# Performance work log

Hardware: AMD Instinct MI355X
Metric: run time of the kernel (lower is better)

## Reference

```python
import jax, jax.numpy as jnp
import numpy as np
from jax import lax

B, C, H, W = 2, 64, 96, 192
D = 48          # max_disp
G = 8           # num_groups
GC = C // G     # group channels
OUT = 32        # out_channels


def conv2d(x, w, pad):
    return lax.conv_general_dilated(x, w, (1, 1), [(pad, pad)] * 2,
                                    dimension_numbers=('NCHW', 'OIHW', 'NCHW'))


def conv3d(x, w, dil, pad):
    return lax.conv_general_dilated(x, w, (1, 1, 1), [(pad, pad)] * 3,
                                    rhs_dilation=(dil, dil, dil),
                                    dimension_numbers=('NCDHW', 'OIDHW', 'NCDHW'))


def setup_inputs() -> dict:
    key = jax.random.key(0)
    ks = jax.random.split(key, 9)
    s = 0.05
    return dict(
        feat_l=jax.random.normal(ks[0], (B, C, H, W), jnp.float32),
        feat_r=jax.random.normal(ks[1], (B, C, H, W), jnp.float32),
        edge_mask=jax.random.uniform(ks[2], (B, 1, H, W), jnp.float32),
        w_pred1=jax.random.normal(ks[3], (32, C + 1, 3, 3), jnp.float32) * s,
        bn_gamma=jnp.ones((32,), jnp.float32),
        bn_beta=jnp.zeros((32,), jnp.float32),
        bn_mean=jnp.zeros((32,), jnp.float32),
        bn_var=jnp.ones((32,), jnp.float32),
        w_pred2=jax.random.normal(ks[4], (3, 32, 1, 1), jnp.float32) * s,
        b_pred2=jnp.zeros((3,), jnp.float32),
        temp=jnp.ones((1,), jnp.float32),
        w_s=jax.random.normal(ks[5], (G, G, 3, 3, 3), jnp.float32) * s,
        w_m=jax.random.normal(ks[6], (G, G, 3, 3, 3), jnp.float32) * s,
        w_l=jax.random.normal(ks[7], (G, G, 3, 3, 3), jnp.float32) * s,
        w_final=jax.random.normal(ks[8], (OUT, G, 1, 1, 1), jnp.float32) * s,
        b_final=jnp.zeros((OUT,), jnp.float32),
    )


def _forward(feat_l, feat_r, edge_mask, w_pred1, bn_gamma, bn_beta, bn_mean,
             bn_var, w_pred2, b_pred2, temp, w_s, w_m, w_l, w_final, b_final):
    # --- group-wise normalized correlation volume ---
    fl = feat_l.reshape(B, G, GC, H, W)
    fr = feat_r.reshape(B, G, GC, H, W)
    eps = 1e-12
    fl = fl / jnp.maximum(jnp.linalg.norm(fl, axis=2, keepdims=True), eps)
    fr = fr / jnp.maximum(jnp.linalg.norm(fr, axis=2, keepdims=True), eps)
    pad = D - 1
    fr_pad = jnp.pad(fr, ((0, 0), (0, 0), (0, 0), (0, 0), (pad, 0)))
    inv = np.float32(1.0 / np.sqrt(GC))

    def body(_, d):
        shifted = lax.dynamic_slice_in_dim(fr_pad, pad - d, W, axis=4)
        corr = jnp.sum(fl * shifted, axis=2) * inv  # [B,G,H,W]
        return None, corr

    _, vols = lax.scan(body, None, jnp.arange(D))          # [D,B,G,H,W]
    base = jnp.transpose(vols, (1, 2, 0, 3, 4))            # [B,G,D,H,W]

    # --- scale predictor (conv -> BN(eval) -> relu -> 1x1 conv) ---
    x = jnp.concatenate([feat_l, edge_mask], axis=1)       # [B,C+1,H,W]
    x = conv2d(x, w_pred1, 1)
    x = (x - bn_mean[:, None, None]) * (bn_gamma[:, None, None]
         / jnp.sqrt(bn_var[:, None, None] + 1e-5)) + bn_beta[:, None, None]
    x = jax.nn.relu(x)
    logits = conv2d(x, w_pred2, 0) + b_pred2[:, None, None]  # [B,3,H,W]
    t = jnp.maximum(temp, 0.1)
    sw = jax.nn.softmax(logits / t, axis=1)
    w_s_exp = sw[:, 0:1, None]   # [B,1,1,H,W]
    w_m_exp = sw[:, 1:2, None]
    w_l_exp = sw[:, 2:3, None]

    # --- multi-dilation 3D aggregation fused by predicted weights ---
    fused = (conv3d(base, w_s, 1, 1) * w_s_exp
             + conv3d(base, w_m, 2, 2) * w_m_exp
             + conv3d(base, w_l, 4, 4) * w_l_exp)
    out = conv3d(fused, w_final, 1, 0) + b_final[None, :, None, None, None]
    return out


def reference(feat_l, feat_r, edge_mask, w_pred1, bn_gamma, bn_beta, bn_mean,
              bn_var, w_pred2, b_pred2, temp, w_s, w_m, w_l, w_final, b_final):
    return _forward(feat_l, feat_r, edge_mask, w_pred1, bn_gamma, bn_beta,
                    bn_mean, bn_var, w_pred2, b_pred2, temp, w_s, w_m, w_l,
                    w_final, b_final)
```

## Files before the change

### kernel.cpp

```cpp
#include <hip/hip_runtime.h>
#include <hip/hip_bf16.h>

#define B_   2
#define C_   64
#define H_   96
#define W_   192
#define D_   48
#define G_   8
#define OUT_ 32
#define HW_  (H_ * W_)

#define DP_ 56
#define HP_ 104
#define WP_ 200
#define PLANE_ (HP_ * WP_ * 8)
#define BASEH_HALFS (B_ * DP_ * PLANE_)

#define OFF_FLN   0
#define OFF_FRN   2359296
#define OFF_BASEH 4718592
#define OFF_SW    14036992
#define OFF_BPACK 14147584
#define OFF_WP1T  14158336

typedef _Float16 f16x8  __attribute__((ext_vector_type(8)));
typedef float    f32x4  __attribute__((ext_vector_type(4)));
typedef float    f32x16 __attribute__((ext_vector_type(16)));

__global__ void wtrans_kernel(const float* __restrict__ w_s,
                              const float* __restrict__ w_m,
                              const float* __restrict__ w_l,
                              const float* __restrict__ w_final,
                              const float* __restrict__ w_pred1,
                              _Float16* __restrict__ bpack,
                              float* __restrict__ wp1T) {
    int i = blockIdx.x * 256 + threadIdx.x;
    if (i < 21504) {
        int j = i & 7;
        int lane = (i >> 3) & 63;
        int kc = i >> 9;
        int c = kc % 14, k = kc / 14;
        int hf = lane >> 5, n = lane & 31;
        int kd = 0, kh = 0, kw = 0; bool valid = true;
        if (c < 9)        { kd = hf ? 1 : -1; kh = c / 3 - 1; kw = c % 3 - 1; }
        else if (c < 12)  { kd = 0; kh = hf ? 1 : -1; kw = (c - 9) - 1; }
        else if (c == 12) { kd = 0; kh = 0; kw = hf ? 1 : -1; }
        else              { valid = (hf == 0); }
        float val = 0.f;
        if (valid) {
            int tap = (kd + 1) * 9 + (kh + 1) * 3 + (kw + 1);
            const float* wsel = (k == 0) ? w_s : (k == 1) ? w_m : w_l;
            #pragma unroll
            for (int g = 0; g < 8; ++g)
                val += w_final[n * 8 + g] * wsel[(g * 8 + j) * 27 + tap];
        }
        bpack[i] = (_Float16)val;
    } else if (i < 21504 + 18720) {
        int j = i - 21504;
        int oc = j & 31; int it = j >> 5; int ic = it / 9; int t = it - ic * 9;
        wp1T[j] = w_pred1[(oc * 65 + ic) * 9 + t];
    }
}

__global__ __launch_bounds__(256) void norm_kernel(const float* __restrict__ feat_l,
                                                   const float* __restrict__ feat_r,
                                                   float* __restrict__ fln,
                                                   float* __restrict__ frn) {
    int hw = blockIdx.x * 256 + threadIdx.x;
    int bg = blockIdx.y;
    const float* src = blockIdx.z ? feat_r : feat_l;
    float*       dst = blockIdx.z ? frn    : fln;
    float v[8]; float s = 0.f;
    #pragma unroll
    for (int c = 0; c < 8; ++c) {
        v[c] = src[(bg * 8 + c) * HW_ + hw];
        s += v[c] * v[c];
    }
    float inv = 1.0f / fmaxf(sqrtf(s), 1e-12f);
    #pragma unroll
    for (int c = 0; c < 8; ++c) dst[((long)bg * HW_ + hw) * 8 + c] = v[c] * inv;
}

__global__ __launch_bounds__(256) void corr_kernel(const float* __restrict__ fln,
                                                   const float* __restrict__ frn,
                                                   _Float16* __restrict__ baseh) {
    int tid = threadIdx.x;
    int g = tid & 7, wi = tid >> 3;
    int w = blockIdx.x * 32 + wi;
    int h = blockIdx.y;
    int b = blockIdx.z;
    const float* flp  = fln + (size_t)((((b * G_ + g) * H_ + h) * W_ + w)) * 8;
    const float* frow = frn + (size_t)((((b * G_ + g) * H_ + h) * W_)) * 8;
    f32x4 a0 = *(const f32x4*)(flp);
    f32x4 a1 = *(const f32x4*)(flp + 4);
    const float inv = 0.35355339059327373f;
    _Float16* dst = baseh + (size_t)((b * DP_ + 4) * HP_ + 4 + h) * WP_ * 8 + (size_t)(4 + w) * 8 + g;
    for (int d = 0; d < D_; ++d) {
        int wd = w - d;
        float acc = 0.f;
        if (wd >= 0) {
            f32x4 b0 = *(const f32x4*)(frow + wd * 8);
            f32x4 b1 = *(const f32x4*)(frow + wd * 8 + 4);
            acc = a0[0]*b0[0] + a0[1]*b0[1] + a0[2]*b0[2] + a0[3]*b0[3]
                + a1[0]*b1[0] + a1[1]*b1[1] + a1[2]*b1[2] + a1[3]*b1[3];
            acc *= inv;
        }
        dst[(size_t)d * PLANE_] = (_Float16)acc;
    }
}

__global__ __launch_bounds__(256) void pred_kernel(const float* __restrict__ feat_l,
                                                   const float* __restrict__ edge,
                                                   const float* __restrict__ wp1T,
                                                   const float* __restrict__ gamma,
                                                   const float* __restrict__ beta,
                                                   const float* __restrict__ mean,
                                                   const float* __restrict__ var,
                                                   const float* __restrict__ w2,
                                                   const float* __restrict__ b2,
                                                   const float* __restrict__ temp,
                                                   float* __restrict__ swp) {
    int pid = blockIdx.x * 256 + threadIdx.x;
    int b = pid / HW_; int hw = pid - b * HW_;
    int h = hw / W_;   int w = hw - h * W_;

    float acc[32];
    #pragma unroll
    for (int i = 0; i < 32; ++i) acc[i] = 0.f;

    for (int ic = 0; ic < 65; ++ic) {
        const float* src = (ic < 64) ? (feat_l + (size_t)(b * 64 + ic) * HW_)
                                     : (edge + (size_t)b * HW_);
        float v[9];
        #pragma unroll
        for (int ky = 0; ky < 3; ++ky) {
            int y = h + ky - 1;
            #pragma unroll
            for (int kx = 0; kx < 3; ++kx) {
                int x = w + kx - 1;
                bool ok = (y >= 0) && (y < H_) && (x >= 0) && (x < W_);
                v[ky * 3 + kx] = ok ? src[y * W_ + x] : 0.f;
            }
        }
        #pragma unroll
        for (int t = 0; t < 9; ++t) {
            const float* wrow = wp1T + (ic * 9 + t) * 32;
            float vv = v[t];
            #pragma unroll
            for (int oc = 0; oc < 32; ++oc) acc[oc] = fmaf(vv, wrow[oc], acc[oc]);
        }
    }

    float l0 = b2[0], l1 = b2[1], l2 = b2[2];
    #pragma unroll
    for (int oc = 0; oc < 32; ++oc) {
        float sc = gamma[oc] / sqrtf(var[oc] + 1e-5f);
        float xb = (acc[oc] - mean[oc]) * sc + beta[oc];
        float r = fmaxf(xb, 0.f);
        l0 = fmaf(w2[0 * 32 + oc], r, l0);
        l1 = fmaf(w2[1 * 32 + oc], r, l1);
        l2 = fmaf(w2[2 * 32 + oc], r, l2);
    }
    float t = fmaxf(temp[0], 0.1f);
    float it = 1.0f / t;
    l0 *= it; l1 *= it; l2 *= it;
    float m = fmaxf(l0, fmaxf(l1, l2));
    float e0 = __expf(l0 - m), e1 = __expf(l1 - m), e2 = __expf(l2 - m);
    float is = 1.0f / (e0 + e1 + e2);
    swp[0 * (B_ * HW_) + pid] = e0 * is;
    swp[1 * (B_ * HW_) + pid] = e1 * is;
    swp[2 * (B_ * HW_) + pid] = e2 * is;
}

__global__ __launch_bounds__(256, 2) void fusedconv_mfma32(
        const _Float16* __restrict__ baseh,
        const float* __restrict__ swp,
        const _Float16* __restrict__ bpack,
        const float* __restrict__ bf,
        float* __restrict__ out) {
    __shared__ _Float16 bsh[3 * 14 * 64 * 8];

    int tid = threadIdx.x;
    {
        const f16x8* srcv = (const f16x8*)bpack;
        f16x8* dstv = (f16x8*)bsh;
        for (int i = tid; i < 2688; i += 256) dstv[i] = srcv[i];
    }

    int L   = blockIdx.x + 6 * (blockIdx.y + 48 * blockIdx.z);
    int sL  = (L & 7) * 144 + (L >> 3);
    int bx  = sL % 6;
    int byz = sL / 6;
    int by  = byz % 48;
    int bz  = byz / 48;

    int wave = tid >> 6, lane = tid & 63;
    int m = lane & 31, hf = lane >> 5;
    int hh = wave >> 1, dh = wave & 1;
    int w0 = bx * 32;
    int h  = by * 2 + hh;
    int b  = bz >> 1;
    int dq = bz & 1;
    int d0 = dq * 24 + dh * 12;

    f16x8 swh[3];
    #pragma unroll
    for (int k = 0; k < 3; ++k) {
        float s = swp[k * (B_ * HW_) + b * HW_ + h * W_ + w0 + m];
        _Float16 hs = (_Float16)s;
        f16x8 t;
        #pragma unroll
        for (int j = 0; j < 8; ++j) t[j] = hs;
        swh[k] = t;
    }

    int hdv[3][4];
    #pragma unroll
    for (int k = 0; k < 3; ++k) {
        int dil = 1 << k;
        hdv[k][0] = hf * (2 * dil * HP_ * WP_ * 8 * 2);
        hdv[k][1] = hf * (2 * dil * WP_ * 8 * 2);
        hdv[k][2] = hf * (2 * dil * 8 * 2);
        hdv[k][3] = 0;
    }

    const char* bb = (const char*)baseh;
    char*       ob = (char*)out;

    unsigned pm = (unsigned)(((((b * DP_ + 4 + d0) * HP_ + 4 + h) * WP_ + 4 + w0 + m) * 8) * 2);
    float bias = bf[m];
    unsigned outoff = (unsigned)((((b * OUT_ + m) * D_ + d0) * HW_ + h * W_ + w0 + 4 * hf) * 4);

    __syncthreads();

    for (int d = 0; d < 12; ++d) {
        unsigned bofs = (unsigned)(lane * 16);
        asm volatile("" : "+v"(bofs));
        const char* bshp = (const char*)bsh + bofs;

        f32x16 acc0, acc1;
        #pragma unroll
        for (int i = 0; i < 16; ++i) { acc0[i] = 0.f; acc1[i] = 0.f; }
        #pragma unroll
        for (int k = 0; k < 3; ++k) {
            int dil = 1 << k;
            #pragma unroll
            for (int c = 0; c < 14; ++c) {
                int coff, cls;
                if (c < 9)        { coff = ((-dil * HP_ + (c / 3 - 1) * dil) * WP_ * 8 + (c % 3 - 1) * dil * 8) * 2; cls = 0; }
                else if (c < 12)  { coff = ((-dil) * WP_ * 8 + ((c - 9) - 1) * dil * 8) * 2;                          cls = 1; }
                else if (c == 12) { coff = -dil * 16;                                                                  cls = 2; }
                else              { coff = 0;                                                                          cls = 3; }
                unsigned a = pm + (unsigned)(hdv[k][cls] + coff);
                f16x8 av = *(const f16x8*)(bb + a);
                f16x8 Bv = *(const f16x8*)(bshp + (k * 14 + c) * 1024);
                av = av * swh[k];
                if (c & 1) acc1 = __builtin_amdgcn_mfma_f32_32x32x16_f16(av, Bv, acc1, 0, 0, 0);
                else       acc0 = __builtin_amdgcn_mfma_f32_32x32x16_f16(av, Bv, acc0, 0, 0, 0);
            }
        }
        #pragma unroll
        for (int q = 0; q < 4; ++q) {
            f32x4 v;
            #pragma unroll
            for (int i = 0; i < 4; ++i) v[i] = acc0[4 * q + i] + acc1[4 * q + i] + bias;
            *(f32x4*)(ob + outoff + q * 32) = v;
        }
        pm += PLANE_ * 2;
        outoff += HW_ * 4;
    }
}

extern "C" void kernel_launch(void* const* d_in, const int* in_sizes, int n_in,
                              void* d_out, int out_size, void* d_ws, size_t ws_size,
                              hipStream_t stream) {
    const float* feat_l   = (const float*)d_in[0];
    const float* feat_r   = (const float*)d_in[1];
    const float* edge     = (const float*)d_in[2];
    const float* w_pred1  = (const float*)d_in[3];
    const float* bn_gamma = (const float*)d_in[4];
    const float* bn_beta  = (const float*)d_in[5];
    const float* bn_mean  = (const float*)d_in[6];
    const float* bn_var   = (const float*)d_in[7];
    const float* w_pred2  = (const float*)d_in[8];
    const float* b_pred2  = (const float*)d_in[9];
    const float* temp     = (const float*)d_in[10];
    const float* w_s      = (const float*)d_in[11];
    const float* w_m      = (const float*)d_in[12];
    const float* w_l      = (const float*)d_in[13];
    const float* w_final  = (const float*)d_in[14];
    const float* b_final  = (const float*)d_in[15];
    float* out = (float*)d_out;

    float* ws = (float*)d_ws;
    float*     fln   = ws + OFF_FLN;
    float*     frn   = ws + OFF_FRN;
    _Float16*  baseh = (_Float16*)(ws + OFF_BASEH);
    float*     swp   = ws + OFF_SW;
    _Float16*  bpack = (_Float16*)(ws + OFF_BPACK);
    float*     wp1T  = ws + OFF_WP1T;

    wtrans_kernel<<<dim3(158), 256, 0, stream>>>(w_s, w_m, w_l, w_final, w_pred1, bpack, wp1T);
    hipMemsetAsync(baseh, 0, (size_t)BASEH_HALFS * sizeof(_Float16), stream);
    norm_kernel<<<dim3(HW_ / 256, B_ * G_, 2), 256, 0, stream>>>(feat_l, feat_r, fln, frn);
    corr_kernel<<<dim3(W_ / 32, H_, B_), 256, 0, stream>>>(fln, frn, baseh);
    pred_kernel<<<dim3(B_ * HW_ / 256), 256, 0, stream>>>(feat_l, edge, wp1T, bn_gamma,
                                                          bn_beta, bn_mean, bn_var,
                                                          w_pred2, b_pred2, temp, swp);
    fusedconv_mfma32<<<dim3(W_ / 32, H_ / 2, B_ * 2), 256, 0, stream>>>(baseh, swp, bpack, b_final, out);
}
```

Measured before the change: 543.9 us.

## Fuse normalization into correlation kernel and double fused-conv block size

```diff
diff --git a/kernel.cpp b/kernel.cpp
--- a/kernel.cpp
+++ b/kernel.cpp
@@ -62,48 +62,51 @@
     }
 }
 
-__global__ __launch_bounds__(256) void norm_kernel(const float* __restrict__ feat_l,
+__global__ __launch_bounds__(256) void corr_kernel(const float* __restrict__ feat_l,
                                                    const float* __restrict__ feat_r,
-                                                   float* __restrict__ fln,
-                                                   float* __restrict__ frn) {
-    int hw = blockIdx.x * 256 + threadIdx.x;
-    int bg = blockIdx.y;
-    const float* src = blockIdx.z ? feat_r : feat_l;
-    float*       dst = blockIdx.z ? frn    : fln;
-    float v[8]; float s = 0.f;
-    #pragma unroll
-    for (int c = 0; c < 8; ++c) {
-        v[c] = src[(bg * 8 + c) * HW_ + hw];
-        s += v[c] * v[c];
-    }
-    float inv = 1.0f / fmaxf(sqrtf(s), 1e-12f);
-    #pragma unroll
-    for (int c = 0; c < 8; ++c) dst[((long)bg * HW_ + hw) * 8 + c] = v[c] * inv;
-}
-
-__global__ __launch_bounds__(256) void corr_kernel(const float* __restrict__ fln,
-                                                   const float* __restrict__ frn,
                                                    _Float16* __restrict__ baseh) {
+    __shared__ float frl[80 * 68];
     int tid = threadIdx.x;
-    int g = tid & 7, wi = tid >> 3;
-    int w = blockIdx.x * 32 + wi;
     int h = blockIdx.y;
     int b = blockIdx.z;
-    const float* flp  = fln + (size_t)((((b * G_ + g) * H_ + h) * W_ + w)) * 8;
-    const float* frow = frn + (size_t)((((b * G_ + g) * H_ + h) * W_)) * 8;
-    f32x4 a0 = *(const f32x4*)(flp);
-    f32x4 a1 = *(const f32x4*)(flp + 4);
-    const float inv = 0.35355339059327373f;
+    int w0 = blockIdx.x * 32;
+    int wbase = w0 - 48;
+
+    for (int p = tid; p < 640; p += 256) {
+        int gg = p / 80;
+        int iw = p - gg * 80;
+        int wg = wbase + iw;
+        if (wg >= 0) {
+            const float* src = feat_r + (size_t)(b * 64 + gg * 8) * HW_ + h * W_ + wg;
+            float v[8]; float s = 0.f;
+            #pragma unroll
+            for (int c = 0; c < 8; ++c) { v[c] = src[(size_t)c * HW_]; s += v[c] * v[c]; }
+            float inv = 0.35355339059327373f / fmaxf(sqrtf(s), 1e-12f);
+            #pragma unroll
+            for (int c = 0; c < 8; ++c) frl[iw * 68 + gg * 8 + c] = v[c] * inv;
+        }
+    }
+
+    int g = tid & 7, wi = tid >> 3;
+    int w = w0 + wi;
+    const float* fls = feat_l + (size_t)(b * 64 + g * 8) * HW_ + h * W_ + w;
+    float a[8]; float s = 0.f;
+    #pragma unroll
+    for (int c = 0; c < 8; ++c) { a[c] = fls[(size_t)c * HW_]; s += a[c] * a[c]; }
+    float inv = 1.0f / fmaxf(sqrtf(s), 1e-12f);
+    #pragma unroll
+    for (int c = 0; c < 8; ++c) a[c] *= inv;
+
+    __syncthreads();
+
     _Float16* dst = baseh + (size_t)((b * DP_ + 4) * HP_ + 4 + h) * WP_ * 8 + (size_t)(4 + w) * 8 + g;
     for (int d = 0; d < D_; ++d) {
         int wd = w - d;
         float acc = 0.f;
         if (wd >= 0) {
-            f32x4 b0 = *(const f32x4*)(frow + wd * 8);
-            f32x4 b1 = *(const f32x4*)(frow + wd * 8 + 4);
-            acc = a0[0]*b0[0] + a0[1]*b0[1] + a0[2]*b0[2] + a0[3]*b0[3]
-                + a1[0]*b1[0] + a1[1]*b1[1] + a1[2]*b1[2] + a1[3]*b1[3];
-            acc *= inv;
+            const float* fr = frl + (wd - wbase) * 68 + g * 8;
+            acc = a[0]*fr[0] + a[1]*fr[1] + a[2]*fr[2] + a[3]*fr[3]
+                + a[4]*fr[4] + a[5]*fr[5] + a[6]*fr[6] + a[7]*fr[7];
         }
         dst[(size_t)d * PLANE_] = (_Float16)acc;
     }
@@ -172,7 +175,7 @@
     swp[2 * (B_ * HW_) + pid] = e2 * is;
 }
 
-__global__ __launch_bounds__(256, 2) void fusedconv_mfma32(
+__global__ __launch_bounds__(512, 2) void fusedconv_mfma32(
         const _Float16* __restrict__ baseh,
         const float* __restrict__ swp,
         const _Float16* __restrict__ bpack,
@@ -184,21 +187,21 @@
     {
         const f16x8* srcv = (const f16x8*)bpack;
         f16x8* dstv = (f16x8*)bsh;
-        for (int i = tid; i < 2688; i += 256) dstv[i] = srcv[i];
-    }
-
-    int L   = blockIdx.x + 6 * (blockIdx.y + 48 * blockIdx.z);
-    int sL  = (L & 7) * 144 + (L >> 3);
+        for (int i = tid; i < 2688; i += 512) dstv[i] = srcv[i];
+    }
+
+    int L   = blockIdx.x + 6 * (blockIdx.y + 24 * blockIdx.z);
+    int sL  = (L & 7) * 72 + (L >> 3);
     int bx  = sL % 6;
-    int byz = sL / 6;
-    int by  = byz % 48;
-    int bz  = byz / 48;
+    int t2  = sL / 6;
+    int by  = t2 % 24;
+    int bz  = t2 / 24;
 
     int wave = tid >> 6, lane = tid & 63;
     int m = lane & 31, hf = lane >> 5;
     int hh = wave >> 1, dh = wave & 1;
     int w0 = bx * 32;
-    int h  = by * 2 + hh;
+    int h  = by * 4 + hh;
     int b  = bz >> 1;
     int dq = bz & 1;
     int d0 = dq * 24 + dh * 12;
@@ -293,8 +296,6 @@
     float* out = (float*)d_out;
 
     float* ws = (float*)d_ws;
-    float*     fln   = ws + OFF_FLN;
-    float*     frn   = ws + OFF_FRN;
     _Float16*  baseh = (_Float16*)(ws + OFF_BASEH);
     float*     swp   = ws + OFF_SW;
     _Float16*  bpack = (_Float16*)(ws + OFF_BPACK);
@@ -302,10 +303,9 @@
 
     wtrans_kernel<<<dim3(158), 256, 0, stream>>>(w_s, w_m, w_l, w_final, w_pred1, bpack, wp1T);
     hipMemsetAsync(baseh, 0, (size_t)BASEH_HALFS * sizeof(_Float16), stream);
-    norm_kernel<<<dim3(HW_ / 256, B_ * G_, 2), 256, 0, stream>>>(feat_l, feat_r, fln, frn);
-    corr_kernel<<<dim3(W_ / 32, H_, B_), 256, 0, stream>>>(fln, frn, baseh);
+    corr_kernel<<<dim3(W_ / 32, H_, B_), 256, 0, stream>>>(feat_l, feat_r, baseh);
     pred_kernel<<<dim3(B_ * HW_ / 256), 256, 0, stream>>>(feat_l, edge, wp1T, bn_gamma,
                                                           bn_beta, bn_mean, bn_var,
                                                           w_pred2, b_pred2, temp, swp);
-    fusedconv_mfma32<<<dim3(W_ / 32, H_ / 2, B_ * 2), 256, 0, stream>>>(baseh, swp, bpack, b_final, out);
-}
+    fusedconv_mfma32<<<dim3(W_ / 32, H_ / 4, B_ * 2), 512, 0, stream>>>(baseh, swp, bpack, b_final, out);
+}
```

New measurement: 533.1 us. -2.0%, faster.
